# Optimization experiments

Hardware: AMD Instinct MI355X
Metric: run time of the kernel (lower is better)

## Reference

```python
import jax, jax.numpy as jnp
import numpy as np

B, N = 16384, 64

def setup_inputs() -> dict:
    key = jax.random.key(0)
    a = jax.random.normal(key, (B, N, N), dtype=jnp.float32)
    # symeig / eigh require symmetric input; symmetrize like SPD inputs would be
    x = 0.5 * (a + jnp.swapaxes(a, -2, -1))
    return {"input": x}

def reference(input) -> jnp.ndarray:
    # s, u = symeig(input); out = u @ diag(exp(s)) @ u^T
    s, u = jnp.linalg.eigh(input)          # s: [B,N], u: [B,N,N]
    # fuse diag_embed + two matmuls: (u * exp(s)) @ u^T
    return jnp.einsum('bik,bk,bjk->bij', u, jnp.exp(s), u)
```

## Files before the change

kernel.cpp:

```cpp
#include <hip/hip_runtime.h>
#include <math.h>

#define NB 64
#define TPB 256

__device__ __constant__ float CF[16] = {
    1.0f,
    1.0f,
    0.5f,
    1.6666666666666666e-01f,
    4.1666666666666664e-02f,
    8.3333333333333332e-03f,
    1.3888888888888889e-03f,
    1.9841269841269841e-04f,
    2.4801587301587302e-05f,
    2.7557319223985893e-06f,
    2.7557319223985888e-07f,
    2.5052108385441720e-08f,
    2.0876756987868100e-09f,
    1.6059043836821613e-10f,
    1.1470745597729725e-11f,
    7.6471637318198164e-13f
};

typedef __attribute__((ext_vector_type(8))) short bf16x8;
typedef __attribute__((ext_vector_type(16))) float f32x16;
typedef __attribute__((ext_vector_type(4))) unsigned int u32x4;

#define MFMA32 __builtin_amdgcn_mfma_f32_32x32x16_bf16

__device__ __forceinline__ void split_pk(float x0, float x1, unsigned& ph, unsigned& pl) {
    unsigned h;
    asm("v_cvt_pk_bf16_f32 %0, %1, %2" : "=v"(h) : "v"(x0), "v"(x1));
    float h0 = __builtin_bit_cast(float, h << 16);
    float h1 = __builtin_bit_cast(float, h & 0xFFFF0000u);
    float r0 = x0 - h0;
    float r1 = x1 - h1;
    unsigned l;
    asm("v_cvt_pk_bf16_f32 %0, %1, %2" : "=v"(l) : "v"(r0), "v"(r1));
    ph = h; pl = l;
}

__device__ __forceinline__ float bf2f(unsigned short h) {
    unsigned u = ((unsigned)h) << 16;
    return __builtin_bit_cast(float, u);
}

__device__ __forceinline__ unsigned swzoff(int row, int byteInRow) {
    return (unsigned)(row * 128 + (byteInRow ^ ((row & 7) << 4)));
}

__device__ __forceinline__ bf16x8 ldfrag(const unsigned short* buf, int row, int f, int lh) {
    const char* p = (const char*)buf + swzoff(row, f * 32 + lh * 16);
    return __builtin_bit_cast(bf16x8, *(const u32x4*)p);
}

__device__ __forceinline__ f32x16 mm3(const bf16x8* ah, const bf16x8* al,
                                      const bf16x8* bh, const bf16x8* bl) {
    f32x16 acc = {};
#pragma unroll
    for (int f = 0; f < 4; ++f) acc = MFMA32(ah[f], bh[f], acc, 0, 0, 0);
#pragma unroll
    for (int f = 0; f < 4; ++f) acc = MFMA32(al[f], bh[f], acc, 0, 0, 0);
#pragma unroll
    for (int f = 0; f < 4; ++f) acc = MFMA32(ah[f], bl[f], acc, 0, 0, 0);
    return acc;
}

__device__ __forceinline__ void store_cT(unsigned short* Bh, unsigned short* Bl,
                                         const float* v, int c_out, int rbase) {
#pragma unroll
    for (int g = 0; g < 4; ++g) {
        uint2 wh, wl;
        split_pk(v[g * 4 + 0], v[g * 4 + 1], wh.x, wl.x);
        split_pk(v[g * 4 + 2], v[g * 4 + 3], wh.y, wl.y);
        unsigned off = swzoff(c_out, (rbase + g * 8) * 2);
        *(uint2*)((char*)Bh + off) = wh;
        *(uint2*)((char*)Bl + off) = wl;
    }
}

__global__ __launch_bounds__(TPB, 4)
void spd_expmap_mfma(const float* __restrict__ in, float* __restrict__ out)
{
    __shared__ __align__(16) unsigned short SB[4 * 4096];
    unsigned short* B0h = SB;
    unsigned short* B0l = SB + 4096;
    unsigned short* B1h = SB + 8192;
    unsigned short* B1l = SB + 12288;
    float* fscratch = (float*)B1h;

    const int tid  = threadIdx.x;
    const int lane = tid & 63;
    const int wv   = tid >> 6;
    const int wr   = (wv >> 1) * 32;
    const int wc   = (wv & 1) * 32;
    const int l31  = lane & 31;
    const int lh   = lane >> 5;
    const int c_out = wc + l31;
    const int rbase = wr + 4 * lh;
    const size_t base = (size_t)blockIdx.x * (NB * NB);
    const bool diag = (wr == wc);

    unsigned dmask = 0;
#pragma unroll
    for (int g = 0; g < 4; ++g)
#pragma unroll
        for (int q = 0; q < 4; ++q)
            if (rbase + g * 8 + q == c_out) dmask |= 1u << (g * 4 + q);

    {
        const int r  = tid >> 2;
        const int cb = (tid & 3) * 16;
        const float4* gp = (const float4*)(in + base) + tid * 4;
        float vv[16];
#pragma unroll
        for (int i = 0; i < 4; ++i) {
            float4 t = gp[i];
            vv[i * 4 + 0] = t.x; vv[i * 4 + 1] = t.y;
            vv[i * 4 + 2] = t.z; vv[i * 4 + 3] = t.w;
        }
        unsigned hw[8], lw[8];
#pragma unroll
        for (int i = 0; i < 8; ++i)
            split_pk(vv[2 * i], vv[2 * i + 1], hw[i], lw[i]);
        u32x4 H0 = {hw[0], hw[1], hw[2], hw[3]}, H1 = {hw[4], hw[5], hw[6], hw[7]};
        u32x4 L0 = {lw[0], lw[1], lw[2], lw[3]}, L1 = {lw[4], lw[5], lw[6], lw[7]};
        unsigned o0 = swzoff(r, cb * 2), o1 = swzoff(r, cb * 2 + 16);
        *(u32x4*)((char*)B0h + o0) = H0; *(u32x4*)((char*)B0h + o1) = H1;
        *(u32x4*)((char*)B0l + o0) = L0; *(u32x4*)((char*)B0l + o1) = L1;
    }
    __syncthreads();

    f32x16 acc;
    {
        bf16x8 ah[4], al[4], bh[4], bl[4];
#pragma unroll
        for (int f = 0; f < 4; ++f) {
            ah[f] = ldfrag(B0h, wr + l31, f, lh);
            al[f] = ldfrag(B0l, wr + l31, f, lh);
        }
        if (diag) {
#pragma unroll
            for (int f = 0; f < 4; ++f) { bh[f] = ah[f]; bl[f] = al[f]; }
        } else {
#pragma unroll
            for (int f = 0; f < 4; ++f) {
                bh[f] = ldfrag(B0h, wc + l31, f, lh);
                bl[f] = ldfrag(B0l, wc + l31, f, lh);
            }
        }
        acc = mm3(ah, al, bh, bl);
        float fr = 0.f;
#pragma unroll
        for (int r = 0; r < 16; ++r) fr += acc[r] * acc[r];
#pragma unroll
        for (int off = 32; off; off >>= 1) fr += __shfl_xor(fr, off);
        if (lane == 0) fscratch[wv] = fr;
    }
    __syncthreads();

    const float total = fscratch[0] + fscratch[1] + fscratch[2] + fscratch[3];
    __syncthreads();
    const float bound = sqrtf(sqrtf(total));
    int sexp = 0;
    if (bound > 4.f) {
        sexp = (int)ceilf(log2f(bound)) - 2;
        if (sexp < 0) sexp = 0;
        if (sexp > 24) sexp = 24;
    }
    const float sc1 = exp2f(-(float)sexp);
    const float sc2 = sc1 * sc1;

    {
        float v[16];
#pragma unroll
        for (int r = 0; r < 16; ++r) v[r] = acc[r] * sc2;
        store_cT(B1h, B1l, v, c_out, rbase);
    }

    float x_out[16];
#pragma unroll
    for (int g = 0; g < 4; ++g) {
        unsigned off = swzoff(c_out, (rbase + g * 8) * 2);
        uint2 xh = *(const uint2*)((const char*)B0h + off);
        uint2 xl = *(const uint2*)((const char*)B0l + off);
        x_out[g * 4 + 0] = (bf2f((unsigned short)(xh.x & 0xFFFF)) + bf2f((unsigned short)(xl.x & 0xFFFF))) * sc1;
        x_out[g * 4 + 1] = (bf2f((unsigned short)(xh.x >> 16))    + bf2f((unsigned short)(xl.x >> 16)))    * sc1;
        x_out[g * 4 + 2] = (bf2f((unsigned short)(xh.y & 0xFFFF)) + bf2f((unsigned short)(xl.y & 0xFFFF))) * sc1;
        x_out[g * 4 + 3] = (bf2f((unsigned short)(xh.y >> 16))    + bf2f((unsigned short)(xl.y >> 16)))    * sc1;
    }

    {
        float v[16];
#pragma unroll
        for (int r = 0; r < 16; ++r)
            v[r] = CF[13] * x_out[r] + (((dmask >> r) & 1) ? CF[12] : 0.f);
        store_cT(B0h, B0l, v, c_out, rbase);
    }
    __syncthreads();

    bf16x8 ya_h[4], ya_l[4];
#pragma unroll
    for (int f = 0; f < 4; ++f) {
        ya_h[f] = ldfrag(B1h, wr + l31, f, lh);
        ya_l[f] = ldfrag(B1l, wr + l31, f, lh);
    }
    __syncthreads();

    unsigned short* curh = B0h; unsigned short* curl = B0l;
    unsigned short* nxth = B1h; unsigned short* nxtl = B1l;
#pragma unroll 1
    for (int j = 5; j >= 0; --j) {
        bf16x8 pbh[4], pbl[4];
#pragma unroll
        for (int f = 0; f < 4; ++f) {
            pbh[f] = ldfrag(curh, wc + l31, f, lh);
            pbl[f] = ldfrag(curl, wc + l31, f, lh);
        }
        f32x16 a2 = mm3(ya_h, ya_l, pbh, pbl);
        float w[16];
        const float cI = CF[2 * j], cX = CF[2 * j + 1];
#pragma unroll
        for (int r = 0; r < 16; ++r)
            w[r] = a2[r] + cX * x_out[r] + (((dmask >> r) & 1) ? cI : 0.f);
        store_cT(nxth, nxtl, w, c_out, rbase);
        unsigned short* th = curh; curh = nxth; nxth = th;
        unsigned short* tl = curl; curl = nxtl; nxtl = tl;
        __syncthreads();
    }

#pragma unroll 1
    for (int t = 0; t < sexp; ++t) {
        bf16x8 pah[4], pal[4], pbh[4], pbl[4];
#pragma unroll
        for (int f = 0; f < 4; ++f) {
            pah[f] = ldfrag(curh, wr + l31, f, lh);
            pal[f] = ldfrag(curl, wr + l31, f, lh);
        }
        if (diag) {
#pragma unroll
            for (int f = 0; f < 4; ++f) { pbh[f] = pah[f]; pbl[f] = pal[f]; }
        } else {
#pragma unroll
            for (int f = 0; f < 4; ++f) {
                pbh[f] = ldfrag(curh, wc + l31, f, lh);
                pbl[f] = ldfrag(curl, wc + l31, f, lh);
            }
        }
        f32x16 a2 = mm3(pah, pal, pbh, pbl);
        if (t == sexp - 1) {
#pragma unroll
            for (int g = 0; g < 4; ++g)
#pragma unroll
                for (int q = 0; q < 4; ++q)
                    out[base + (size_t)(rbase + g * 8 + q) * NB + c_out] = a2[g * 4 + q];
        } else {
            store_cT(nxth, nxtl, (const float*)&a2, c_out, rbase);
            unsigned short* th = curh; curh = nxth; nxth = th;
            unsigned short* tl = curl; curl = nxtl; nxtl = tl;
            __syncthreads();
        }
    }

    if (sexp == 0) {
#pragma unroll
        for (int g = 0; g < 4; ++g) {
            unsigned off = swzoff(c_out, (rbase + g * 8) * 2);
            uint2 ph = *(const uint2*)((const char*)curh + off);
            uint2 pl = *(const uint2*)((const char*)curl + off);
            float v0 = bf2f((unsigned short)(ph.x & 0xFFFF)) + bf2f((unsigned short)(pl.x & 0xFFFF));
            float v1 = bf2f((unsigned short)(ph.x >> 16))    + bf2f((unsigned short)(pl.x >> 16));
            float v2 = bf2f((unsigned short)(ph.y & 0xFFFF)) + bf2f((unsigned short)(pl.y & 0xFFFF));
            float v3 = bf2f((unsigned short)(ph.y >> 16))    + bf2f((unsigned short)(pl.y >> 16));
            out[base + (size_t)(rbase + g * 8 + 0) * NB + c_out] = v0;
            out[base + (size_t)(rbase + g * 8 + 1) * NB + c_out] = v1;
            out[base + (size_t)(rbase + g * 8 + 2) * NB + c_out] = v2;
            out[base + (size_t)(rbase + g * 8 + 3) * NB + c_out] = v3;
        }
    }
}

extern "C" void kernel_launch(void* const* d_in, const int* in_sizes, int n_in,
                              void* d_out, int out_size, void* d_ws, size_t ws_size,
                              hipStream_t stream) {
    const float* in = reinterpret_cast<const float*>(d_in[0]);
    float* out = reinterpret_cast<float*>(d_out);
    const int nmat = in_sizes[0] / (NB * NB);
    hipLaunchKernelGGL(spd_expmap_mfma, dim3(nmat), dim3(TPB), 0, stream, in, out);
}
```

Before: 306.6 us.

## Halve LDS footprint by single-buffering matrices with extra barriers

Replaces the double-buffered hi/lo bf16 LDS buffers with a single buffer pair (16KB instead of 32KB). Fragments are read into registers before a barrier, then overwritten in place, which needs extra __syncthreads per iteration. The diagonal mask becomes a float select array so the update folds into FMAs. The goal is higher occupancy from lower LDS use, paid for with more barriers and longer register lifetimes.

```diff
diff --git a/kernel.cpp b/kernel.cpp
--- a/kernel.cpp
+++ b/kernel.cpp
@@ -83,12 +83,10 @@
 __global__ __launch_bounds__(TPB, 4)
 void spd_expmap_mfma(const float* __restrict__ in, float* __restrict__ out)
 {
-    __shared__ __align__(16) unsigned short SB[4 * 4096];
-    unsigned short* B0h = SB;
-    unsigned short* B0l = SB + 4096;
-    unsigned short* B1h = SB + 8192;
-    unsigned short* B1l = SB + 12288;
-    float* fscratch = (float*)B1h;
+    __shared__ __align__(16) unsigned short SB[2 * 4096];
+    __shared__ float fscratch[4];
+    unsigned short* Bh = SB;
+    unsigned short* Bl = SB + 4096;
 
     const int tid  = threadIdx.x;
     const int lane = tid & 63;
@@ -102,12 +100,12 @@
     const size_t base = (size_t)blockIdx.x * (NB * NB);
     const bool diag = (wr == wc);
 
-    unsigned dmask = 0;
+    float dsel[16];
 #pragma unroll
     for (int g = 0; g < 4; ++g)
 #pragma unroll
         for (int q = 0; q < 4; ++q)
-            if (rbase + g * 8 + q == c_out) dmask |= 1u << (g * 4 + q);
+            dsel[g * 4 + q] = (rbase + g * 8 + q == c_out) ? 1.0f : 0.0f;
 
     {
         const int r  = tid >> 2;
@@ -127,8 +125,8 @@
         u32x4 H0 = {hw[0], hw[1], hw[2], hw[3]}, H1 = {hw[4], hw[5], hw[6], hw[7]};
         u32x4 L0 = {lw[0], lw[1], lw[2], lw[3]}, L1 = {lw[4], lw[5], lw[6], lw[7]};
         unsigned o0 = swzoff(r, cb * 2), o1 = swzoff(r, cb * 2 + 16);
-        *(u32x4*)((char*)B0h + o0) = H0; *(u32x4*)((char*)B0h + o1) = H1;
-        *(u32x4*)((char*)B0l + o0) = L0; *(u32x4*)((char*)B0l + o1) = L1;
+        *(u32x4*)((char*)Bh + o0) = H0; *(u32x4*)((char*)Bh + o1) = H1;
+        *(u32x4*)((char*)Bl + o0) = L0; *(u32x4*)((char*)Bl + o1) = L1;
     }
     __syncthreads();
 
@@ -137,8 +135,8 @@
         bf16x8 ah[4], al[4], bh[4], bl[4];
 #pragma unroll
         for (int f = 0; f < 4; ++f) {
-            ah[f] = ldfrag(B0h, wr + l31, f, lh);
-            al[f] = ldfrag(B0l, wr + l31, f, lh);
+            ah[f] = ldfrag(Bh, wr + l31, f, lh);
+            al[f] = ldfrag(Bl, wr + l31, f, lh);
         }
         if (diag) {
 #pragma unroll
@@ -146,8 +144,8 @@
         } else {
 #pragma unroll
             for (int f = 0; f < 4; ++f) {
-                bh[f] = ldfrag(B0h, wc + l31, f, lh);
-                bl[f] = ldfrag(B0l, wc + l31, f, lh);
+                bh[f] = ldfrag(Bh, wc + l31, f, lh);
+                bl[f] = ldfrag(Bl, wc + l31, f, lh);
             }
         }
         acc = mm3(ah, al, bh, bl);
@@ -158,10 +156,21 @@
         for (int off = 32; off; off >>= 1) fr += __shfl_xor(fr, off);
         if (lane == 0) fscratch[wv] = fr;
     }
+
+    float x_out[16];
+#pragma unroll
+    for (int g = 0; g < 4; ++g) {
+        unsigned off = swzoff(c_out, (rbase + g * 8) * 2);
+        uint2 xh = *(const uint2*)((const char*)Bh + off);
+        uint2 xl = *(const uint2*)((const char*)Bl + off);
+        x_out[g * 4 + 0] = bf2f((unsigned short)(xh.x & 0xFFFF)) + bf2f((unsigned short)(xl.x & 0xFFFF));
+        x_out[g * 4 + 1] = bf2f((unsigned short)(xh.x >> 16))    + bf2f((unsigned short)(xl.x >> 16));
+        x_out[g * 4 + 2] = bf2f((unsigned short)(xh.y & 0xFFFF)) + bf2f((unsigned short)(xl.y & 0xFFFF));
+        x_out[g * 4 + 3] = bf2f((unsigned short)(xh.y >> 16))    + bf2f((unsigned short)(xl.y >> 16));
+    }
     __syncthreads();
 
     const float total = fscratch[0] + fscratch[1] + fscratch[2] + fscratch[3];
-    __syncthreads();
     const float bound = sqrtf(sqrtf(total));
     int sexp = 0;
     if (bound > 4.f) {
@@ -171,112 +180,96 @@
     }
     const float sc1 = exp2f(-(float)sexp);
     const float sc2 = sc1 * sc1;
+#pragma unroll
+    for (int r = 0; r < 16; ++r) x_out[r] *= sc1;
 
     {
         float v[16];
 #pragma unroll
         for (int r = 0; r < 16; ++r) v[r] = acc[r] * sc2;
-        store_cT(B1h, B1l, v, c_out, rbase);
-    }
-
-    float x_out[16];
-#pragma unroll
-    for (int g = 0; g < 4; ++g) {
-        unsigned off = swzoff(c_out, (rbase + g * 8) * 2);
-        uint2 xh = *(const uint2*)((const char*)B0h + off);
-        uint2 xl = *(const uint2*)((const char*)B0l + off);
-        x_out[g * 4 + 0] = (bf2f((unsigned short)(xh.x & 0xFFFF)) + bf2f((unsigned short)(xl.x & 0xFFFF))) * sc1;
-        x_out[g * 4 + 1] = (bf2f((unsigned short)(xh.x >> 16))    + bf2f((unsigned short)(xl.x >> 16)))    * sc1;
-        x_out[g * 4 + 2] = (bf2f((unsigned short)(xh.y & 0xFFFF)) + bf2f((unsigned short)(xl.y & 0xFFFF))) * sc1;
-        x_out[g * 4 + 3] = (bf2f((unsigned short)(xh.y >> 16))    + bf2f((unsigned short)(xl.y >> 16)))    * sc1;
-    }
+        store_cT(Bh, Bl, v, c_out, rbase);
+    }
+    __syncthreads();
+
+    bf16x8 ya_h[4], ya_l[4];
+#pragma unroll
+    for (int f = 0; f < 4; ++f) {
+        ya_h[f] = ldfrag(Bh, wr + l31, f, lh);
+        ya_l[f] = ldfrag(Bl, wr + l31, f, lh);
+    }
+    __syncthreads();
 
     {
         float v[16];
 #pragma unroll
         for (int r = 0; r < 16; ++r)
-            v[r] = CF[13] * x_out[r] + (((dmask >> r) & 1) ? CF[12] : 0.f);
-        store_cT(B0h, B0l, v, c_out, rbase);
-    }
-    __syncthreads();
-
-    bf16x8 ya_h[4], ya_l[4];
-#pragma unroll
-    for (int f = 0; f < 4; ++f) {
-        ya_h[f] = ldfrag(B1h, wr + l31, f, lh);
-        ya_l[f] = ldfrag(B1l, wr + l31, f, lh);
-    }
-    __syncthreads();
-
-    unsigned short* curh = B0h; unsigned short* curl = B0l;
-    unsigned short* nxth = B1h; unsigned short* nxtl = B1l;
+            v[r] = fmaf(dsel[r], CF[12], CF[13] * x_out[r]);
+        store_cT(Bh, Bl, v, c_out, rbase);
+    }
+    __syncthreads();
+
 #pragma unroll 1
     for (int j = 5; j >= 0; --j) {
         bf16x8 pbh[4], pbl[4];
 #pragma unroll
         for (int f = 0; f < 4; ++f) {
-            pbh[f] = ldfrag(curh, wc + l31, f, lh);
-            pbl[f] = ldfrag(curl, wc + l31, f, lh);
-        }
+            pbh[f] = ldfrag(Bh, wc + l31, f, lh);
+            pbl[f] = ldfrag(Bl, wc + l31, f, lh);
+        }
+        __syncthreads();
         f32x16 a2 = mm3(ya_h, ya_l, pbh, pbl);
         float w[16];
         const float cI = CF[2 * j], cX = CF[2 * j + 1];
 #pragma unroll
         for (int r = 0; r < 16; ++r)
-            w[r] = a2[r] + cX * x_out[r] + (((dmask >> r) & 1) ? cI : 0.f);
-        store_cT(nxth, nxtl, w, c_out, rbase);
-        unsigned short* th = curh; curh = nxth; nxth = th;
-        unsigned short* tl = curl; curl = nxtl; nxtl = tl;
+            w[r] = fmaf(dsel[r], cI, fmaf(cX, x_out[r], a2[r]));
+        store_cT(Bh, Bl, w, c_out, rbase);
         __syncthreads();
-    }
-
-#pragma unroll 1
-    for (int t = 0; t < sexp; ++t) {
-        bf16x8 pah[4], pal[4], pbh[4], pbl[4];
-#pragma unroll
-        for (int f = 0; f < 4; ++f) {
-            pah[f] = ldfrag(curh, wr + l31, f, lh);
-            pal[f] = ldfrag(curl, wr + l31, f, lh);
-        }
-        if (diag) {
-#pragma unroll
-            for (int f = 0; f < 4; ++f) { pbh[f] = pah[f]; pbl[f] = pal[f]; }
-        } else {
-#pragma unroll
-            for (int f = 0; f < 4; ++f) {
-                pbh[f] = ldfrag(curh, wc + l31, f, lh);
-                pbl[f] = ldfrag(curl, wc + l31, f, lh);
-            }
-        }
-        f32x16 a2 = mm3(pah, pal, pbh, pbl);
-        if (t == sexp - 1) {
-#pragma unroll
-            for (int g = 0; g < 4; ++g)
-#pragma unroll
-                for (int q = 0; q < 4; ++q)
-                    out[base + (size_t)(rbase + g * 8 + q) * NB + c_out] = a2[g * 4 + q];
-        } else {
-            store_cT(nxth, nxtl, (const float*)&a2, c_out, rbase);
-            unsigned short* th = curh; curh = nxth; nxth = th;
-            unsigned short* tl = curl; curl = nxtl; nxtl = tl;
-            __syncthreads();
-        }
     }
 
     if (sexp == 0) {
 #pragma unroll
         for (int g = 0; g < 4; ++g) {
             unsigned off = swzoff(c_out, (rbase + g * 8) * 2);
-            uint2 ph = *(const uint2*)((const char*)curh + off);
-            uint2 pl = *(const uint2*)((const char*)curl + off);
-            float v0 = bf2f((unsigned short)(ph.x & 0xFFFF)) + bf2f((unsigned short)(pl.x & 0xFFFF));
-            float v1 = bf2f((unsigned short)(ph.x >> 16))    + bf2f((unsigned short)(pl.x >> 16));
-            float v2 = bf2f((unsigned short)(ph.y & 0xFFFF)) + bf2f((unsigned short)(pl.y & 0xFFFF));
-            float v3 = bf2f((unsigned short)(ph.y >> 16))    + bf2f((unsigned short)(pl.y >> 16));
-            out[base + (size_t)(rbase + g * 8 + 0) * NB + c_out] = v0;
-            out[base + (size_t)(rbase + g * 8 + 1) * NB + c_out] = v1;
-            out[base + (size_t)(rbase + g * 8 + 2) * NB + c_out] = v2;
-            out[base + (size_t)(rbase + g * 8 + 3) * NB + c_out] = v3;
+            uint2 ph = *(const uint2*)((const char*)Bh + off);
+            uint2 pl = *(const uint2*)((const char*)Bl + off);
+            out[base + (size_t)(rbase + g * 8 + 0) * NB + c_out] = bf2f((unsigned short)(ph.x & 0xFFFF)) + bf2f((unsigned short)(pl.x & 0xFFFF));
+            out[base + (size_t)(rbase + g * 8 + 1) * NB + c_out] = bf2f((unsigned short)(ph.x >> 16))    + bf2f((unsigned short)(pl.x >> 16));
+            out[base + (size_t)(rbase + g * 8 + 2) * NB + c_out] = bf2f((unsigned short)(ph.y & 0xFFFF)) + bf2f((unsigned short)(pl.y & 0xFFFF));
+            out[base + (size_t)(rbase + g * 8 + 3) * NB + c_out] = bf2f((unsigned short)(ph.y >> 16))    + bf2f((unsigned short)(pl.y >> 16));
+        }
+    } else {
+#pragma unroll 1
+        for (int t = 0; t < sexp; ++t) {
+            bf16x8 pah[4], pal[4], pbh[4], pbl[4];
+#pragma unroll
+            for (int f = 0; f < 4; ++f) {
+                pah[f] = ldfrag(Bh, wr + l31, f, lh);
+                pal[f] = ldfrag(Bl, wr + l31, f, lh);
+            }
+            if (diag) {
+#pragma unroll
+                for (int f = 0; f < 4; ++f) { pbh[f] = pah[f]; pbl[f] = pal[f]; }
+            } else {
+#pragma unroll
+                for (int f = 0; f < 4; ++f) {
+                    pbh[f] = ldfrag(Bh, wc + l31, f, lh);
+                    pbl[f] = ldfrag(Bl, wc + l31, f, lh);
+                }
+            }
+            if (t == sexp - 1) {
+                f32x16 a2 = mm3(pah, pal, pbh, pbl);
+#pragma unroll
+                for (int g = 0; g < 4; ++g)
+#pragma unroll
+                    for (int q = 0; q < 4; ++q)
+                        out[base + (size_t)(rbase + g * 8 + q) * NB + c_out] = a2[g * 4 + q];
+            } else {
+                __syncthreads();
+                f32x16 a2 = mm3(pah, pal, pbh, pbl);
+                store_cT(Bh, Bl, (const float*)&a2, c_out, rbase);
+                __syncthreads();
+            }
         }
     }
 }
```

Result: slower. 321.6 us (+4.9%).
